# Kernel tuning notes

Measured on AMD Instinct MI355X. Metric: run time of the kernel, lower is better.

## Reference

```python
import jax, jax.numpy as jnp
import numpy as np

ROPE_BASE = 1000000.0
EPS = 1e-6
N_HEADS = 16

def apply_rope(x, base=ROPE_BASE):
    # x: [b, seq, heads, head_dim]
    b, seq, n_heads, dim = x.shape
    half = dim // 2
    i = jnp.arange(half)
    theta = 1.0 / base ** (2 * i / dim)
    pos = jnp.arange(seq)
    angles = pos[:, None] * theta[None, :]            # [seq, half]
    cos = jnp.cos(angles)[None, :, None, :]
    sin = jnp.sin(angles)[None, :, None, :]
    x1, x2 = jnp.split(x, 2, axis=-1)
    return jnp.concatenate([x1 * cos - x2 * sin, x1 * sin + x2 * cos], axis=-1)

def setup_inputs() -> dict:
    key = jax.random.key(0)
    ks = jax.random.split(key, 6)
    b, seq, dim = 2, 2048, 1024
    scale = 1.0 / np.sqrt(dim)
    return {
        "x": jax.random.normal(ks[0], (b, seq, dim), dtype=jnp.float32),
        "norm_scale": jnp.ones((dim,), dtype=jnp.float32),
        "Wq": jax.random.normal(ks[1], (dim, dim), dtype=jnp.float32) * scale,
        "Wk": jax.random.normal(ks[2], (dim, dim), dtype=jnp.float32) * scale,
        "Wv": jax.random.normal(ks[3], (dim, dim), dtype=jnp.float32) * scale,
        "Wo": jax.random.normal(ks[4], (dim, dim), dtype=jnp.float32) * scale,
    }

def reference(x, norm_scale, Wq, Wk, Wv, Wo):
    b, seq, d = x.shape
    n_heads = N_HEADS
    dh = d // n_heads
    # RMSNorm
    var = jnp.mean(jnp.square(x), axis=-1, keepdims=True)
    x_norm = x * jax.lax.rsqrt(var + EPS) * norm_scale
    # QKV projections ([in,out] weights as in nnx.Linear)
    q = (x_norm @ Wq).reshape(b, seq, n_heads, dh)
    k = (x_norm @ Wk).reshape(b, seq, n_heads, dh)
    v = (x_norm @ Wv).reshape(b, seq, n_heads, dh)
    q = apply_rope(q)
    k = apply_rope(k)
    # causal attention with explicit score matrix (faithful to source)
    scores = jnp.einsum('bthd,bshd->bhts', q, k) / jnp.sqrt(jnp.float32(dh))
    causal = jnp.triu(jnp.full((seq, seq), -jnp.inf, dtype=jnp.float32), k=1)
    scores = scores + causal[None, None, :, :]
    weights = jax.nn.softmax(scores, axis=-1)
    out = jnp.einsum('bhts,bshd->bthd', weights, v).reshape(b, seq, d)
    return out @ Wo
```

## Files before the change

kernel.cpp:

```cpp
#include <hip/hip_runtime.h>

typedef unsigned short ushort_t;
typedef __attribute__((ext_vector_type(8))) short short8;
typedef __attribute__((ext_vector_type(4))) float floatx4;

#define DEV static __device__ __forceinline__
#define NEG_BIG (-1e30f)

typedef const __attribute__((address_space(1))) unsigned int* gas_ptr;
typedef __attribute__((address_space(3))) unsigned int* las_ptr;

DEV void async16(const ushort_t* g, ushort_t* l) {
    __builtin_amdgcn_global_load_lds((gas_ptr)(const void*)g, (las_ptr)(void*)l, 16, 0, 0);
}

DEV float bf2f(ushort_t u) {
    union { unsigned u; float f; } v; v.u = ((unsigned)u) << 16; return v.f;
}
DEV ushort_t f2bf(float f) {
    union { float f; unsigned u; } v; v.f = f;
    unsigned r = v.u + 0x7FFF + ((v.u >> 16) & 1);
    return (ushort_t)(r >> 16);
}
DEV float load_bf16_scrub(const ushort_t* p, size_t i) {
    ushort_t u = p[i];
    if (((u >> 7) & 0xFF) == 0xFF) u = 0;
    return bf2f(u);
}
DEV float load_f32_scrub(const ushort_t* p, size_t i) {
    unsigned u = ((const unsigned*)p)[i];
    if (((u >> 23) & 0xFF) == 0xFF) u = 0;
    union { unsigned u; float f; } v; v.u = u; return v.f;
}

DEV int probe_is_f32(const ushort_t* __restrict__ p) {
    int tid = threadIdx.x + threadIdx.y * blockDim.x;
    int nthr = blockDim.x * blockDim.y;
    __shared__ int cnt;
    if (tid == 0) cnt = 0;
    __syncthreads();
    int weird = 0;
    for (int i = tid; i < 2048; i += nthr) {
        unsigned e = (p[i] >> 7) & 0xFF;
        weird += (e >= 0x90) ? 1 : 0;
    }
#pragma unroll
    for (int off = 32; off; off >>= 1) weird += __shfl_xor(weird, off);
    if ((tid & 63) == 0) atomicAdd(&cnt, weird);
    __syncthreads();
    return cnt > 16;
}

__global__ void prep_kernel(const ushort_t* __restrict__ W0,
                            const ushort_t* __restrict__ W1,
                            const ushort_t* __restrict__ W2,
                            const ushort_t* __restrict__ W3,
                            ushort_t* __restrict__ WTq3,
                            ushort_t* __restrict__ WoT,
                            const ushort_t* __restrict__ x,
                            const ushort_t* __restrict__ g,
                            ushort_t* __restrict__ xn) {
    int is_f32 = probe_is_f32(x);
    int z = blockIdx.z;
    if (z < 4) {
        const ushort_t* W = (z == 0) ? W0 : (z == 1) ? W1 : (z == 2) ? W2 : W3;
        __shared__ ushort_t tile[32][33];
        int tx = threadIdx.x, ty = threadIdx.y;
        int xx = blockIdx.x * 32 + tx;
        int y0 = blockIdx.y * 32;
#pragma unroll
        for (int j = 0; j < 32; j += 8) {
            size_t idx = (size_t)(y0 + ty + j) * 1024 + xx;
            tile[ty + j][tx] = f2bf(is_f32 ? load_f32_scrub(W, idx) : load_bf16_scrub(W, idx));
        }
        __syncthreads();
        int nx = blockIdx.y * 32 + tx;
        ushort_t* dst = (z < 3) ? WTq3 : WoT;
        int ny0 = blockIdx.x * 32 + ((z < 3) ? z * 1024 : 0);
#pragma unroll
        for (int j = 0; j < 32; j += 8)
            dst[(size_t)(ny0 + ty + j) * 1024 + nx] = tile[tx][ty + j];
    } else {
        int row = (z - 4) * 1024 + blockIdx.y * 32 + blockIdx.x;
        int tid = threadIdx.y * 32 + threadIdx.x;
        float vals[4], gv[4];
        size_t base = (size_t)row * 1024 + tid * 4;
#pragma unroll
        for (int i = 0; i < 4; i++) {
            if (is_f32) {
                vals[i] = load_f32_scrub(x, base + i);
                gv[i]   = load_f32_scrub(g, tid * 4 + i);
            } else {
                vals[i] = load_bf16_scrub(x, base + i);
                gv[i]   = load_bf16_scrub(g, tid * 4 + i);
            }
        }
        float ss = vals[0]*vals[0] + vals[1]*vals[1] + vals[2]*vals[2] + vals[3]*vals[3];
#pragma unroll
        for (int off = 32; off > 0; off >>= 1) ss += __shfl_xor(ss, off);
        __shared__ float red[4];
        if ((tid & 63) == 0) red[tid >> 6] = ss;
        __syncthreads();
        ss = red[0] + red[1] + red[2] + red[3];
        float inv = rsqrtf(ss * (1.0f / 1024.0f) + 1e-6f);
#pragma unroll
        for (int i = 0; i < 4; i++)
            xn[base + i] = f2bf(vals[i] * inv * gv[i]);
    }
}

__global__ __launch_bounds__(256, 4) void gemm_qkv(const ushort_t* __restrict__ A,
                                                   const ushort_t* __restrict__ Bt,
                                                   ushort_t* __restrict__ qb,
                                                   ushort_t* __restrict__ kb,
                                                   ushort_t* __restrict__ vt) {
    const int K = 1024;
    int tid = threadIdx.x;
    int lane = tid & 63, w = tid >> 6;
    int c = lane & 15, quad = lane >> 4;
    int mh = w >> 1, nh = w & 1;
    int lin = blockIdx.y * gridDim.x + blockIdx.x;
    int xcd = lin & 7, idx = lin >> 3;
    int bm = ((xcd & 3) * 8 + (idx & 7)) * 128;
    int bn = ((xcd >> 2) * 12 + (idx >> 3)) * 128;
    int lr = lane >> 2, lq = lane & 3;

    __shared__ __align__(16) ushort_t As[16 * 512];
    __shared__ __align__(16) ushort_t Bs[16 * 512];

    const floatx4 zero = {0.f, 0.f, 0.f, 0.f};
    floatx4 acc[4][4];
#pragma unroll
    for (int i = 0; i < 4; i++)
#pragma unroll
        for (int j = 0; j < 4; j++) acc[i][j] = zero;

    for (int k0 = 0; k0 < K; k0 += 64) {
        __syncthreads();
#pragma unroll
        for (int ci = 0; ci < 8; ci++) {
            int ch = w * 8 + ci;
            if (ch < 16) {
                int rg = ch >> 1, kc = ch & 1;
                async16(A + (size_t)(bm + rg * 16 + lr) * K + k0 + kc * 32 + lq * 8,
                        As + ch * 512);
            } else {
                int b2 = ch - 16;
                int rg = b2 >> 1, kc = b2 & 1;
                async16(Bt + (size_t)(bn + rg * 16 + lr) * K + k0 + kc * 32 + lq * 8,
                        Bs + b2 * 512);
            }
        }
        __syncthreads();
#pragma unroll
        for (int kc = 0; kc < 2; kc++) {
            short8 af[4], bf[4];
#pragma unroll
            for (int i = 0; i < 4; i++)
                af[i] = *(const short8*)(As + ((mh * 4 + i) * 2 + kc) * 512 + c * 32 + quad * 8);
#pragma unroll
            for (int j = 0; j < 4; j++)
                bf[j] = *(const short8*)(Bs + ((nh * 4 + j) * 2 + kc) * 512 + c * 32 + quad * 8);
#pragma unroll
            for (int i = 0; i < 4; i++)
#pragma unroll
                for (int j = 0; j < 4; j++)
                    acc[i][j] = __builtin_amdgcn_mfma_f32_16x16x32_bf16(af[i], bf[j], acc[i][j], 0, 0, 0);
        }
    }

    int proj = bn >> 10;
    int n0 = (bn & 1023) + nh * 64;
    if (proj < 2) {
        float th0 = exp2f((float)c * (-19.931568569324174f / 32.0f));
        float th1 = exp2f((float)(16 + c) * (-19.931568569324174f / 32.0f));
        float scale = (proj == 0) ? 0.125f : 1.0f;
#pragma unroll
        for (int i = 0; i < 4; i++)
#pragma unroll
            for (int r = 0; r < 4; r++) {
                int s = (bm + mh * 64 + i * 16 + quad * 4 + r) & 2047;
                float sn0, cs0, sn1, cs1;
                sincosf((float)s * th0, &sn0, &cs0);
                sincosf((float)s * th1, &sn1, &cs1);
                float x1a = acc[i][0][r], x2a = acc[i][2][r];
                acc[i][0][r] = (x1a * cs0 - x2a * sn0) * scale;
                acc[i][2][r] = (x1a * sn0 + x2a * cs0) * scale;
                float x1b = acc[i][1][r], x2b = acc[i][3][r];
                acc[i][1][r] = (x1b * cs1 - x2b * sn1) * scale;
                acc[i][3][r] = (x1b * sn1 + x2b * cs1) * scale;
            }
    }
    ushort_t* dst = (proj == 0) ? qb : kb;
#pragma unroll
    for (int i = 0; i < 4; i++)
#pragma unroll
        for (int j = 0; j < 4; j++)
#pragma unroll
            for (int r = 0; r < 4; r++) {
                int row = bm + mh * 64 + i * 16 + quad * 4 + r;
                int col = n0 + j * 16 + c;
                if (proj == 2) {
                    int b = row >> 11, s = row & 2047;
                    int hh = col >> 6, dh = col & 63;
                    vt[(size_t)((b * 16 + hh) * 64 + dh) * 2048 + s] = f2bf(acc[i][j][r]);
                } else {
                    dst[(size_t)row * 1024 + col] = f2bf(acc[i][j][r]);
                }
            }
}

__global__ __launch_bounds__(256, 4) void gemm_out(const ushort_t* __restrict__ A,
                                                   const ushort_t* __restrict__ Bt,
                                                   float* __restrict__ C) {
    const int K = 1024, N = 1024;
    int tid = threadIdx.x;
    int lane = tid & 63, w = tid >> 6;
    int c = lane & 15, quad = lane >> 4;
    int mh = w >> 1, nh = w & 1;
    int lin = blockIdx.y * gridDim.x + blockIdx.x;
    int xcd = lin & 7, idx = lin >> 3;
    int bm = ((xcd & 3) * 8 + (idx & 7)) * 128;
    int bn = ((xcd >> 2) * 8 + (idx >> 3)) * 64;
    int lr = lane >> 2, lq = lane & 3;

    __shared__ __align__(16) ushort_t As[16 * 512];
    __shared__ __align__(16) ushort_t Bs[8 * 512];

    const floatx4 zero = {0.f, 0.f, 0.f, 0.f};
    floatx4 acc[4][2];
#pragma unroll
    for (int i = 0; i < 4; i++)
#pragma unroll
        for (int j = 0; j < 2; j++) acc[i][j] = zero;

    for (int k0 = 0; k0 < K; k0 += 64) {
        __syncthreads();
#pragma unroll
        for (int ci = 0; ci < 6; ci++) {
            int ch = w * 6 + ci;
            if (ch < 16) {
                int rg = ch >> 1, kc = ch & 1;
                async16(A + (size_t)(bm + rg * 16 + lr) * K + k0 + kc * 32 + lq * 8,
                        As + ch * 512);
            } else {
                int b2 = ch - 16;
                int rg = b2 >> 1, kc = b2 & 1;
                async16(Bt + (size_t)(bn + rg * 16 + lr) * K + k0 + kc * 32 + lq * 8,
                        Bs + b2 * 512);
            }
        }
        __syncthreads();
#pragma unroll
        for (int kc = 0; kc < 2; kc++) {
            short8 af[4], bf[2];
#pragma unroll
            for (int i = 0; i < 4; i++)
                af[i] = *(const short8*)(As + ((mh * 4 + i) * 2 + kc) * 512 + c * 32 + quad * 8);
#pragma unroll
            for (int j = 0; j < 2; j++)
                bf[j] = *(const short8*)(Bs + ((nh * 2 + j) * 2 + kc) * 512 + c * 32 + quad * 8);
#pragma unroll
            for (int i = 0; i < 4; i++)
#pragma unroll
                for (int j = 0; j < 2; j++)
                    acc[i][j] = __builtin_amdgcn_mfma_f32_16x16x32_bf16(af[i], bf[j], acc[i][j], 0, 0, 0);
        }
    }
#pragma unroll
    for (int i = 0; i < 4; i++)
#pragma unroll
        for (int j = 0; j < 2; j++)
#pragma unroll
            for (int r = 0; r < 4; r++) {
                int row = bm + mh * 64 + i * 16 + quad * 4 + r;
                int col = bn + nh * 32 + j * 16 + c;
                C[(size_t)row * N + col] = acc[i][j][r];
            }
}

__global__ __launch_bounds__(256) void attn_kernel(const ushort_t* __restrict__ q,
                                                   const ushort_t* __restrict__ k,
                                                   const ushort_t* __restrict__ vt,
                                                   ushort_t* __restrict__ o) {
    int tid = threadIdx.x;
    int lane = tid & 63, w = tid >> 6;
    int c = lane & 15, quad = lane >> 4;
    int bh = blockIdx.x;
    int b = bh >> 4, h = bh & 15;
    int pair = blockIdx.y;
    int lr = lane >> 2, lq = lane & 3;
    const ushort_t* qb  = q + (size_t)b * 2048 * 1024 + h * 64;
    const ushort_t* kbp = k + (size_t)b * 2048 * 1024 + h * 64;
    const ushort_t* vtb = vt + (size_t)(b * 16 + h) * 64 * 2048;
    ushort_t* ob = o + (size_t)b * 2048 * 1024 + h * 64;

    __shared__ __align__(16) ushort_t Ks[8 * 512];
    __shared__ __align__(16) ushort_t Vs[8 * 512];
    __shared__ __align__(16) ushort_t Ps[64 * 72];

    const floatx4 zero = {0.f, 0.f, 0.f, 0.f};

#pragma unroll
    for (int g = 0; g < 2; g++) {
        int qt  = g ? (31 - pair) : pair;
        int t0b = qt * 64;
        int t0w = t0b + w * 16;
        int ntile = qt + 1;

        const ushort_t* qrow = qb + (size_t)(t0w + c) * 1024;
        short8 aq0 = *(const short8*)(qrow + quad * 8);
        short8 aq1 = *(const short8*)(qrow + 32 + quad * 8);

        float l_part[4];
        floatx4 oacc[4];
#pragma unroll
        for (int r = 0; r < 4; r++) l_part[r] = 0.f;
#pragma unroll
        for (int dt = 0; dt < 4; dt++) oacc[dt] = zero;

        for (int kt = 0; kt < ntile; kt++) {
            int s0 = kt * 64;
            __syncthreads();
#pragma unroll
            for (int ci = 0; ci < 4; ci++) {
                int ch = w * 4 + ci;
                if (ch < 8) {
                    int nt = ch >> 1, hf = ch & 1;
                    async16(kbp + (size_t)(s0 + nt * 16 + lr) * 1024 + hf * 32 + lq * 8,
                            Ks + ch * 512);
                } else {
                    int dt = (ch - 8) >> 1, hf = ch & 1;
                    async16(vtb + (size_t)(dt * 16 + lr) * 2048 + s0 + hf * 32 + lq * 8,
                            Vs + (ch - 8) * 512);
                }
            }
            __syncthreads();

            floatx4 sacc[4];
#pragma unroll
            for (int nt = 0; nt < 4; nt++) sacc[nt] = zero;
#pragma unroll
            for (int nt = 0; nt < 4; nt++) {
                short8 b0 = *(const short8*)(Ks + nt * 1024 + c * 32 + quad * 8);
                short8 b1 = *(const short8*)(Ks + nt * 1024 + 512 + c * 32 + quad * 8);
                sacc[nt] = __builtin_amdgcn_mfma_f32_16x16x32_bf16(aq0, b0, sacc[nt], 0, 0, 0);
                sacc[nt] = __builtin_amdgcn_mfma_f32_16x16x32_bf16(aq1, b1, sacc[nt], 0, 0, 0);
            }

            if (kt == ntile - 1) {
#pragma unroll
                for (int r = 0; r < 4; r++) {
                    int t = t0w + quad * 4 + r;
                    float ps = 0.f;
#pragma unroll
                    for (int nt = 0; nt < 4; nt++) {
                        float v = (s0 + nt * 16 + c > t) ? NEG_BIG : sacc[nt][r];
                        float e = __expf(v);
                        ps += e;
                        Ps[(w * 16 + quad * 4 + r) * 72 + nt * 16 + c] = f2bf(e);
                    }
                    l_part[r] += ps;
                }
            } else {
#pragma unroll
                for (int r = 0; r < 4; r++) {
                    float ps = 0.f;
#pragma unroll
                    for (int nt = 0; nt < 4; nt++) {
                        float e = __expf(sacc[nt][r]);
                        ps += e;
                        Ps[(w * 16 + quad * 4 + r) * 72 + nt * 16 + c] = f2bf(e);
                    }
                    l_part[r] += ps;
                }
            }

            short8 pa0 = *(const short8*)(Ps + (w * 16 + c) * 72 + quad * 8);
            short8 pa1 = *(const short8*)(Ps + (w * 16 + c) * 72 + 32 + quad * 8);
#pragma unroll
            for (int dt = 0; dt < 4; dt++) {
                short8 v0 = *(const short8*)(Vs + dt * 1024 + c * 32 + quad * 8);
                short8 v1 = *(const short8*)(Vs + dt * 1024 + 512 + c * 32 + quad * 8);
                oacc[dt] = __builtin_amdgcn_mfma_f32_16x16x32_bf16(pa0, v0, oacc[dt], 0, 0, 0);
                oacc[dt] = __builtin_amdgcn_mfma_f32_16x16x32_bf16(pa1, v1, oacc[dt], 0, 0, 0);
            }
        }

        float linv[4];
#pragma unroll
        for (int r = 0; r < 4; r++) {
            float l = l_part[r];
#pragma unroll
            for (int off = 1; off < 16; off <<= 1) l += __shfl_xor(l, off);
            linv[r] = 1.0f / l;
        }
#pragma unroll
        for (int dt = 0; dt < 4; dt++)
#pragma unroll
            for (int r = 0; r < 4; r++) {
                int t = t0w + quad * 4 + r;
                ob[(size_t)t * 1024 + dt * 16 + c] = f2bf(oacc[dt][r] * linv[r]);
            }
    }
}

extern "C" void kernel_launch(void* const* d_in, const int* in_sizes, int n_in,
                              void* d_out, int out_size, void* d_ws, size_t ws_size,
                              hipStream_t stream) {
    const ushort_t* x  = (const ushort_t*)d_in[0];
    const ushort_t* g  = (const ushort_t*)d_in[1];
    const ushort_t* Wq = (const ushort_t*)d_in[2];
    const ushort_t* Wk = (const ushort_t*)d_in[3];
    const ushort_t* Wv = (const ushort_t*)d_in[4];
    const ushort_t* Wo = (const ushort_t*)d_in[5];

    char* ws = (char*)d_ws;
    const size_t MB = 1ull << 20;
    ushort_t* xn   = (ushort_t*)(ws);
    ushort_t* qb   = (ushort_t*)(ws + 8 * MB);
    ushort_t* kb   = (ushort_t*)(ws + 16 * MB);
    ushort_t* vt   = (ushort_t*)(ws + 24 * MB);
    ushort_t* WTq3 = (ushort_t*)(ws + 32 * MB);
    ushort_t* WoT  = (ushort_t*)(ws + 38 * MB);
    ushort_t* at   = xn;

    prep_kernel<<<dim3(32, 32, 8), dim3(32, 8), 0, stream>>>(Wq, Wk, Wv, Wo, WTq3, WoT, x, g, xn);

    gemm_qkv<<<dim3(24, 32), 256, 0, stream>>>(xn, WTq3, qb, kb, vt);

    attn_kernel<<<dim3(32, 16), 256, 0, stream>>>(qb, kb, vt, at);

    gemm_out<<<dim3(16, 32), 256, 0, stream>>>(at, WoT, (float*)d_out);
}
```

Measured before the change: 212.5 us.

## Double-buffer K/V tiles in attention, vectorize V^T stores, use fast sin/cos

The attention kernel now ping-pongs between two K/V shared-memory buffers. It prefetches the next key/value tile while computing on the current one, which removes one barrier per iteration and hides global-load latency. The QKV GEMM epilogue packs four bf16 values into one 8-byte store for the transposed V output, replacing scattered 2-byte stores. It also swaps sincosf for the __sinf/__cosf intrinsics in RoPE. The costs are doubled K/V LDS usage, which may lower occupancy, and reduced sin/cos accuracy at large angles.

```diff
diff --git a/kernel.cpp b/kernel.cpp
--- a/kernel.cpp
+++ b/kernel.cpp
@@ -2,6 +2,7 @@
 
 typedef unsigned short ushort_t;
 typedef __attribute__((ext_vector_type(8))) short short8;
+typedef __attribute__((ext_vector_type(4))) short short4v;
 typedef __attribute__((ext_vector_type(4))) float floatx4;
 
 #define DEV static __device__ __forceinline__
@@ -180,9 +181,9 @@
 #pragma unroll
             for (int r = 0; r < 4; r++) {
                 int s = (bm + mh * 64 + i * 16 + quad * 4 + r) & 2047;
-                float sn0, cs0, sn1, cs1;
-                sincosf((float)s * th0, &sn0, &cs0);
-                sincosf((float)s * th1, &sn1, &cs1);
+                float a0 = (float)s * th0, a1 = (float)s * th1;
+                float sn0 = __sinf(a0), cs0 = __cosf(a0);
+                float sn1 = __sinf(a1), cs1 = __cosf(a1);
                 float x1a = acc[i][0][r], x2a = acc[i][2][r];
                 acc[i][0][r] = (x1a * cs0 - x2a * sn0) * scale;
                 acc[i][2][r] = (x1a * sn0 + x2a * cs0) * scale;
@@ -190,24 +191,32 @@
                 acc[i][1][r] = (x1b * cs1 - x2b * sn1) * scale;
                 acc[i][3][r] = (x1b * sn1 + x2b * cs1) * scale;
             }
-    }
-    ushort_t* dst = (proj == 0) ? qb : kb;
-#pragma unroll
-    for (int i = 0; i < 4; i++)
-#pragma unroll
-        for (int j = 0; j < 4; j++)
-#pragma unroll
-            for (int r = 0; r < 4; r++) {
-                int row = bm + mh * 64 + i * 16 + quad * 4 + r;
+        ushort_t* dst = (proj == 0) ? qb : kb;
+#pragma unroll
+        for (int i = 0; i < 4; i++)
+#pragma unroll
+            for (int j = 0; j < 4; j++)
+#pragma unroll
+                for (int r = 0; r < 4; r++) {
+                    int row = bm + mh * 64 + i * 16 + quad * 4 + r;
+                    dst[(size_t)row * 1024 + n0 + j * 16 + c] = f2bf(acc[i][j][r]);
+                }
+    } else {
+#pragma unroll
+        for (int i = 0; i < 4; i++) {
+            int row0 = bm + mh * 64 + i * 16 + quad * 4;
+            int b = row0 >> 11, s0v = row0 & 2047;
+#pragma unroll
+            for (int j = 0; j < 4; j++) {
                 int col = n0 + j * 16 + c;
-                if (proj == 2) {
-                    int b = row >> 11, s = row & 2047;
-                    int hh = col >> 6, dh = col & 63;
-                    vt[(size_t)((b * 16 + hh) * 64 + dh) * 2048 + s] = f2bf(acc[i][j][r]);
-                } else {
-                    dst[(size_t)row * 1024 + col] = f2bf(acc[i][j][r]);
-                }
-            }
+                int hh = col >> 6, dh = col & 63;
+                short4v pk;
+#pragma unroll
+                for (int r = 0; r < 4; r++) pk[r] = (short)f2bf(acc[i][j][r]);
+                *(short4v*)(vt + (size_t)((b * 16 + hh) * 64 + dh) * 2048 + s0v) = pk;
+            }
+        }
+    }
 }
 
 __global__ __launch_bounds__(256, 4) void gemm_out(const ushort_t* __restrict__ A,
@@ -295,8 +304,8 @@
     const ushort_t* vtb = vt + (size_t)(b * 16 + h) * 64 * 2048;
     ushort_t* ob = o + (size_t)b * 2048 * 1024 + h * 64;
 
-    __shared__ __align__(16) ushort_t Ks[8 * 512];
-    __shared__ __align__(16) ushort_t Vs[8 * 512];
+    __shared__ __align__(16) ushort_t Ks[2][8 * 512];
+    __shared__ __align__(16) ushort_t Vs[2][8 * 512];
     __shared__ __align__(16) ushort_t Ps[64 * 72];
 
     const floatx4 zero = {0.f, 0.f, 0.f, 0.f};
@@ -319,31 +328,50 @@
 #pragma unroll
         for (int dt = 0; dt < 4; dt++) oacc[dt] = zero;
 
+        __syncthreads();
+#pragma unroll
+        for (int ci = 0; ci < 4; ci++) {
+            int ch = w * 4 + ci;
+            if (ch < 8) {
+                int nt = ch >> 1, hf = ch & 1;
+                async16(kbp + (size_t)(nt * 16 + lr) * 1024 + hf * 32 + lq * 8,
+                        Ks[0] + ch * 512);
+            } else {
+                int dt = (ch - 8) >> 1, hf = ch & 1;
+                async16(vtb + (size_t)(dt * 16 + lr) * 2048 + hf * 32 + lq * 8,
+                        Vs[0] + (ch - 8) * 512);
+            }
+        }
+
         for (int kt = 0; kt < ntile; kt++) {
+            __syncthreads();
+            int cur = kt & 1;
+            if (kt + 1 < ntile) {
+                int s1 = (kt + 1) * 64;
+                int nxt = cur ^ 1;
+#pragma unroll
+                for (int ci = 0; ci < 4; ci++) {
+                    int ch = w * 4 + ci;
+                    if (ch < 8) {
+                        int nt = ch >> 1, hf = ch & 1;
+                        async16(kbp + (size_t)(s1 + nt * 16 + lr) * 1024 + hf * 32 + lq * 8,
+                                Ks[nxt] + ch * 512);
+                    } else {
+                        int dt = (ch - 8) >> 1, hf = ch & 1;
+                        async16(vtb + (size_t)(dt * 16 + lr) * 2048 + s1 + hf * 32 + lq * 8,
+                                Vs[nxt] + (ch - 8) * 512);
+                    }
+                }
+            }
             int s0 = kt * 64;
-            __syncthreads();
-#pragma unroll
-            for (int ci = 0; ci < 4; ci++) {
-                int ch = w * 4 + ci;
-                if (ch < 8) {
-                    int nt = ch >> 1, hf = ch & 1;
-                    async16(kbp + (size_t)(s0 + nt * 16 + lr) * 1024 + hf * 32 + lq * 8,
-                            Ks + ch * 512);
-                } else {
-                    int dt = (ch - 8) >> 1, hf = ch & 1;
-                    async16(vtb + (size_t)(dt * 16 + lr) * 2048 + s0 + hf * 32 + lq * 8,
-                            Vs + (ch - 8) * 512);
-                }
-            }
-            __syncthreads();
 
             floatx4 sacc[4];
 #pragma unroll
             for (int nt = 0; nt < 4; nt++) sacc[nt] = zero;
 #pragma unroll
             for (int nt = 0; nt < 4; nt++) {
-                short8 b0 = *(const short8*)(Ks + nt * 1024 + c * 32 + quad * 8);
-                short8 b1 = *(const short8*)(Ks + nt * 1024 + 512 + c * 32 + quad * 8);
+                short8 b0 = *(const short8*)(Ks[cur] + nt * 1024 + c * 32 + quad * 8);
+                short8 b1 = *(const short8*)(Ks[cur] + nt * 1024 + 512 + c * 32 + quad * 8);
                 sacc[nt] = __builtin_amdgcn_mfma_f32_16x16x32_bf16(aq0, b0, sacc[nt], 0, 0, 0);
                 sacc[nt] = __builtin_amdgcn_mfma_f32_16x16x32_bf16(aq1, b1, sacc[nt], 0, 0, 0);
             }
@@ -380,8 +408,8 @@
             short8 pa1 = *(const short8*)(Ps + (w * 16 + c) * 72 + 32 + quad * 8);
 #pragma unroll
             for (int dt = 0; dt < 4; dt++) {
-                short8 v0 = *(const short8*)(Vs + dt * 1024 + c * 32 + quad * 8);
-                short8 v1 = *(const short8*)(Vs + dt * 1024 + 512 + c * 32 + quad * 8);
+                short8 v0 = *(const short8*)(Vs[cur] + dt * 1024 + c * 32 + quad * 8);
+                short8 v1 = *(const short8*)(Vs[cur] + dt * 1024 + 512 + c * 32 + quad * 8);
                 oacc[dt] = __builtin_amdgcn_mfma_f32_16x16x32_bf16(pa0, v0, oacc[dt], 0, 0, 0);
                 oacc[dt] = __builtin_amdgcn_mfma_f32_16x16x32_bf16(pa1, v1, oacc[dt], 0, 0, 0);
             }
```

Result: faster. 187.3 us (-11.9%).
